# Kernel tuning notes

Measured on AMD Instinct MI355X. Metric: run time of the kernel, lower is better.

## Reference

```python
import jax, jax.numpy as jnp
import numpy as np

B, S = 16, 8192
Q_DIM, K_DIM, ATTN_DIM = 512, 512, 512


def setup_inputs() -> dict:
    key = jax.random.key(0)
    k1, k2, k3, k4, k5, k6 = jax.random.split(key, 6)
    query = jax.random.normal(k1, (B, Q_DIM), dtype=jnp.float32)
    keys = jax.random.normal(k2, (B, S, K_DIM), dtype=jnp.float32)
    mask = jax.random.randint(k3, (B, S), 0, 2, dtype=jnp.int32)
    # learned params (torch Linear stores weight as [out, in]; we keep [in, out])
    Wq = jax.random.normal(k4, (Q_DIM, ATTN_DIM), dtype=jnp.float32) / np.sqrt(Q_DIM)
    Wk = jax.random.normal(k5, (K_DIM, ATTN_DIM), dtype=jnp.float32) / np.sqrt(K_DIM)
    v = jax.random.normal(k6, (ATTN_DIM,), dtype=jnp.float32) / np.sqrt(ATTN_DIM)
    return {"query": query, "keys": keys, "mask": mask, "Wq": Wq, "Wk": Wk, "v": v}


def reference(query, keys, mask, Wq, Wk, v):
    # q: [B, 1, A], k: [B, S, A]
    q = (query @ Wq)[:, None, :]
    k = jnp.einsum('bsk,ka->bsa', keys, Wk)
    # scores e: [B, S]  (v-projection reduces attn dim)
    e = jnp.einsum('bsa,a->bs', jnp.tanh(q + k), v)
    neg_min = jnp.finfo(e.dtype).min
    e = jnp.where(mask == 0, neg_min, e)
    a = jax.nn.softmax(e, axis=-1)  # [B, S]
    c = jnp.einsum('bs,bsk->bk', a, keys)  # context [B, K_DIM]
    return (c, a)
```

## Files before the change

kernel.cpp:

```cpp
#include <hip/hip_runtime.h>

#define BB 16
#define SS 8192
#define DD 512

typedef float  f32x4  __attribute__((ext_vector_type(4)));
typedef __bf16 bf16x8 __attribute__((ext_vector_type(8)));
typedef __bf16 bf16x4 __attribute__((ext_vector_type(4)));

__device__ __forceinline__ void cvt_store_bf4(unsigned short* dst, f32x4 v) {
    bf16x4 o;
    o.x = (__bf16)v.x; o.y = (__bf16)v.y; o.z = (__bf16)v.z; o.w = (__bf16)v.w;
    *(bf16x4*)dst = o;
}

__device__ __forceinline__ float tanh_fast(float x) {
    float e2 = __expf(2.0f * x);
    return 1.0f - 2.0f / (e2 + 1.0f);
}

__global__ void prep_kernel(const float* __restrict__ query, const float* __restrict__ Wq,
                            const float* __restrict__ Wk, float* __restrict__ qproj,
                            unsigned short* __restrict__ WkT)
{
    const int bid = blockIdx.x, t = threadIdx.x;
    if (bid < DD) {
        const int n = bid;
        for (int k = t; k < DD; k += 256) {
            __bf16 h = (__bf16)Wk[k * DD + n];
            WkT[n * DD + k] = __builtin_bit_cast(unsigned short, h);
        }
    } else {
        const int idx = (bid - DD) * 256 + t;
        const int b = idx >> 9;
        const int n = idx & 511;
        const float* q  = query + b * DD;
        const float* wp = Wq + n;
        float acc = 0.0f;
#pragma unroll 8
        for (int k = 0; k < DD; ++k)
            acc = fmaf(q[k], wp[(size_t)k * DD], acc);
        qproj[b * DD + n] = acc;
    }
}

__global__ __launch_bounds__(256, 2) void fused_kernel(
    const float* __restrict__ keys, const unsigned short* __restrict__ WkT,
    const float* __restrict__ qproj, const float* __restrict__ vvec,
    const int* __restrict__ mask, float* __restrict__ e_ws,
    float* __restrict__ cpart, float2* __restrict__ ml_ws)
{
    __shared__ unsigned short ksA[16 * 2048];
    __shared__ float sm_part[4][64];
    __shared__ float w_sh[64];
    __shared__ f32x4 red[128];

    const int tid  = threadIdx.x;
    const int w    = tid >> 6;
    const int lane = tid & 63;
    const int ml   = lane & 15;
    const int quad = lane >> 4;
    const int bid  = blockIdx.x;
    const int b    = bid >> 7;
    const int chunk = bid & 127;
    const int s0   = chunk << 6;

    const int m  = tid >> 2;
    const int q4 = tid & 3;
    const float* krow = keys + ((size_t)(b * SS + s0 + m)) * DD + q4 * 4;
    const int it  = m >> 4;
    const int g0  = q4 >> 1;
    const int j0  = (q4 & 1) * 4;
    const int base0 = it * 512 + ((m & 15) + 16 * g0)       * 8 + j0;
    const int base1 = it * 512 + ((m & 15) + 16 * (g0 + 2)) * 8 + j0;
#pragma unroll 4
    for (int j = 0; j < 16; ++j) {
        f32x4 k0 = *(const f32x4*)(krow + j * 32);
        f32x4 k1 = *(const f32x4*)(krow + j * 32 + 16);
        cvt_store_bf4(&ksA[j * 2048 + base0], k0);
        cvt_store_bf4(&ksA[j * 2048 + base1], k1);
    }
    __syncthreads();

    const unsigned short* wb = WkT + (size_t)(w * 128 + ml) * DD + quad * 8;

    f32x4 acc[4][8];
#pragma unroll
    for (int i = 0; i < 4; ++i)
#pragma unroll
        for (int jn = 0; jn < 8; ++jn) acc[i][jn] = (f32x4){0.f, 0.f, 0.f, 0.f};

#pragma unroll 2
    for (int j = 0; j < 16; ++j) {
        bf16x8 af[4];
#pragma unroll
        for (int i = 0; i < 4; ++i)
            af[i] = *(const bf16x8*)&ksA[j * 2048 + (i * 64 + lane) * 8];
#pragma unroll
        for (int jn = 0; jn < 8; ++jn) {
            bf16x8 bfr = *(const bf16x8*)(wb + (size_t)jn * 16 * DD + j * 32);
#pragma unroll
            for (int i = 0; i < 4; ++i)
                acc[i][jn] = __builtin_amdgcn_mfma_f32_16x16x32_bf16(af[i], bfr, acc[i][jn], 0, 0, 0);
        }
    }

    float qv[8], vv[8];
#pragma unroll
    for (int jn = 0; jn < 8; ++jn) {
        const int n = w * 128 + jn * 16 + ml;
        qv[jn] = qproj[b * DD + n];
        vv[jn] = vvec[n];
    }
#pragma unroll
    for (int i = 0; i < 4; ++i) {
#pragma unroll
        for (int r = 0; r < 4; ++r) {
            float s = 0.0f;
#pragma unroll
            for (int jn = 0; jn < 8; ++jn) {
                float xx = acc[i][jn][r] + qv[jn];
                s += tanh_fast(xx) * vv[jn];
            }
            s += __shfl_xor(s, 1, 64);
            s += __shfl_xor(s, 2, 64);
            s += __shfl_xor(s, 4, 64);
            s += __shfl_xor(s, 8, 64);
            if (ml == 0) sm_part[w][i * 16 + quad * 4 + r] = s;
        }
    }
    __syncthreads();

    if (tid < 64) {
        float e = sm_part[0][tid] + sm_part[1][tid] + sm_part[2][tid] + sm_part[3][tid];
        const int mk = mask[b * SS + s0 + tid];
        if (mk == 0) e = -3.402823466e38f;
        e_ws[(size_t)b * SS + s0 + tid] = e;
        float mx = e;
#pragma unroll
        for (int off = 32; off >= 1; off >>= 1) mx = fmaxf(mx, __shfl_xor(mx, off, 64));
        float wv = (mk == 0) ? 0.0f : __expf(e - mx);
        float l  = wv;
#pragma unroll
        for (int off = 32; off >= 1; off >>= 1) l += __shfl_xor(l, off, 64);
        w_sh[tid] = wv;
        if (tid == 0) ml_ws[b * 128 + chunk] = make_float2(mx, l);
    }
    __syncthreads();

    const int n4 = (tid & 127) << 2;
    const int sh = tid >> 7;
    const float* kctx = keys + ((size_t)(b * SS + s0 + sh * 32)) * DD + n4;
    f32x4 cacc = (f32x4){0.f, 0.f, 0.f, 0.f};
#pragma unroll 8
    for (int sI = 0; sI < 32; ++sI) {
        float wgt = w_sh[sh * 32 + sI];
        f32x4 kv  = *(const f32x4*)(kctx + (size_t)sI * DD);
        cacc += kv * wgt;
    }
    if (sh == 1) red[tid & 127] = cacc;
    __syncthreads();
    if (sh == 0) {
        cacc += red[tid];
        *(f32x4*)(cpart + ((size_t)(b * 128 + chunk)) * 512 + n4) = cacc;
    }
}

__global__ __launch_bounds__(256) void finalize_kernel(
    const float* __restrict__ e_ws, const float* __restrict__ cpart,
    const float2* __restrict__ ml_ws, float* __restrict__ out)
{
    __shared__ float rm[4], rs[4];
    __shared__ float sc_sh[128];
    const int bid = blockIdx.x, t = threadIdx.x;
    const int b = (bid < 16) ? bid : ((bid - 16) >> 3);

    float mi = -3.402823466e38f, li = 0.0f;
    if (t < 128) { float2 p = ml_ws[b * 128 + t]; mi = p.x; li = p.y; }
    float mr = mi;
#pragma unroll
    for (int off = 32; off >= 1; off >>= 1) mr = fmaxf(mr, __shfl_xor(mr, off, 64));
    if ((t & 63) == 0) rm[t >> 6] = mr;
    __syncthreads();
    const float M = fmaxf(fmaxf(rm[0], rm[1]), fmaxf(rm[2], rm[3]));
    float si = (t < 128) ? li * __expf(mi - M) : 0.0f;
#pragma unroll
    for (int off = 32; off >= 1; off >>= 1) si += __shfl_xor(si, off, 64);
    if ((t & 63) == 0) rs[t >> 6] = si;
    __syncthreads();
    const float L = rs[0] + rs[1] + rs[2] + rs[3];
    const float invL = 1.0f / L;

    if (bid < 16) {
        if (t < 128) sc_sh[t] = __expf(ml_ws[b * 128 + t].x - M);
        __syncthreads();
        const int n0 = t * 2;
        float a0 = 0.0f, a1 = 0.0f;
#pragma unroll 4
        for (int i = 0; i < 128; ++i) {
            const float sc = sc_sh[i];
            const float* cp = cpart + ((size_t)(b * 128 + i)) * 512 + n0;
            a0 = fmaf(cp[0], sc, a0);
            a1 = fmaf(cp[1], sc, a1);
        }
        out[b * DD + n0]     = a0 * invL;
        out[b * DD + n0 + 1] = a1 * invL;
    } else {
        const int chunk8 = (bid - 16) & 7;
        const float* ep = e_ws + (size_t)b * SS + chunk8 * 1024;
        float* ap = out + BB * DD + (size_t)b * SS + chunk8 * 1024;
#pragma unroll
        for (int r = 0; r < 4; ++r) {
            float e = ep[t + 256 * r];
            ap[t + 256 * r] = __expf(e - M) * invL;
        }
    }
}

extern "C" void kernel_launch(void* const* d_in, const int* in_sizes, int n_in,
                              void* d_out, int out_size, void* d_ws, size_t ws_size,
                              hipStream_t stream)
{
    const float* query = (const float*)d_in[0];
    const float* keys  = (const float*)d_in[1];
    const int*   mask  = (const int*)  d_in[2];
    const float* Wq    = (const float*)d_in[3];
    const float* Wk    = (const float*)d_in[4];
    const float* v     = (const float*)d_in[5];
    float* out = (float*)d_out;

    float*          qproj = (float*)d_ws;
    unsigned short* WkT   = (unsigned short*)((char*)d_ws + 32768);
    float*          e_ws  = (float*)((char*)d_ws + 32768 + 524288);
    float*          cpart = (float*)((char*)d_ws + 32768 + 2 * 524288);
    float2*         ml_ws = (float2*)((char*)d_ws + 32768 + 2 * 524288 + 4194304);

    prep_kernel    <<<DD + 32, 256, 0, stream>>>(query, Wq, Wk, qproj, WkT);
    fused_kernel   <<<BB * (SS / 64), 256, 0, stream>>>(keys, WkT, qproj, v, mask,
                                                        e_ws, cpart, ml_ws);
    finalize_kernel<<<16 + 128, 256, 0, stream>>>(e_ws, cpart, ml_ws, out);
}
```

Baseline: 560.4 us.

## Widen fused kernel to 512 threads, tile Wk transpose, split finalize reduction

The fused kernel moves from 256 to 512 threads per block, with eight waves each taking 64 of the attention columns. This halves per-thread accumulators and adds an extra reduction stage for the scores and the context partials. The prep kernel now transposes Wk through a 64x64 LDS tile with vectorized loads and stores instead of strided per-element accesses. The finalize context reduction is split across four waves with an LDS combine. The larger blocks aim for more parallelism per block and less register pressure, at the cost of more partial-sum traffic and a declared occupancy that may not be reachable.

```diff
diff --git a/kernel.cpp b/kernel.cpp
--- a/kernel.cpp
+++ b/kernel.cpp
@@ -19,19 +19,32 @@
     return 1.0f - 2.0f / (e2 + 1.0f);
 }
 
-__global__ void prep_kernel(const float* __restrict__ query, const float* __restrict__ Wq,
-                            const float* __restrict__ Wk, float* __restrict__ qproj,
-                            unsigned short* __restrict__ WkT)
-{
+__global__ __launch_bounds__(256) void prep_kernel(
+    const float* __restrict__ query, const float* __restrict__ Wq,
+    const float* __restrict__ Wk, float* __restrict__ qproj,
+    unsigned short* __restrict__ WkT)
+{
+    __shared__ __bf16 lt[64][65];
     const int bid = blockIdx.x, t = threadIdx.x;
-    if (bid < DD) {
-        const int n = bid;
-        for (int k = t; k < DD; k += 256) {
-            __bf16 h = (__bf16)Wk[k * DD + n];
-            WkT[n * DD + k] = __builtin_bit_cast(unsigned short, h);
+    if (bid < 64) {
+        const int k0 = (bid >> 3) * 64, n0 = (bid & 7) * 64;
+#pragma unroll
+        for (int rep = 0; rep < 4; ++rep) {
+            const int k = rep * 16 + (t >> 4), n = (t & 15) * 4;
+            f32x4 vv = *(const f32x4*)&Wk[(size_t)(k0 + k) * DD + n0 + n];
+            lt[k][n] = (__bf16)vv.x; lt[k][n + 1] = (__bf16)vv.y;
+            lt[k][n + 2] = (__bf16)vv.z; lt[k][n + 3] = (__bf16)vv.w;
+        }
+        __syncthreads();
+#pragma unroll
+        for (int rep = 0; rep < 4; ++rep) {
+            const int n = rep * 16 + (t >> 4), k = (t & 15) * 4;
+            bf16x4 o;
+            o.x = lt[k][n]; o.y = lt[k + 1][n]; o.z = lt[k + 2][n]; o.w = lt[k + 3][n];
+            *(bf16x4*)&WkT[(size_t)(n0 + n) * DD + k0 + k] = o;
         }
     } else {
-        const int idx = (bid - DD) * 256 + t;
+        const int idx = (bid - 64) * 256 + t;
         const int b = idx >> 9;
         const int n = idx & 511;
         const float* q  = query + b * DD;
@@ -44,16 +57,16 @@
     }
 }
 
-__global__ __launch_bounds__(256, 2) void fused_kernel(
+__global__ __launch_bounds__(512, 4) void fused_kernel(
     const float* __restrict__ keys, const unsigned short* __restrict__ WkT,
     const float* __restrict__ qproj, const float* __restrict__ vvec,
     const int* __restrict__ mask, float* __restrict__ e_ws,
     float* __restrict__ cpart, float2* __restrict__ ml_ws)
 {
     __shared__ unsigned short ksA[16 * 2048];
-    __shared__ float sm_part[4][64];
+    __shared__ float sm_part[8][64];
     __shared__ float w_sh[64];
-    __shared__ f32x4 red[128];
+    __shared__ f32x4 red[3][128];
 
     const int tid  = threadIdx.x;
     const int w    = tid >> 6;
@@ -65,39 +78,36 @@
     const int chunk = bid & 127;
     const int s0   = chunk << 6;
 
-    const int m  = tid >> 2;
-    const int q4 = tid & 3;
-    const float* krow = keys + ((size_t)(b * SS + s0 + m)) * DD + q4 * 4;
-    const int it  = m >> 4;
-    const int g0  = q4 >> 1;
-    const int j0  = (q4 & 1) * 4;
-    const int base0 = it * 512 + ((m & 15) + 16 * g0)       * 8 + j0;
-    const int base1 = it * 512 + ((m & 15) + 16 * (g0 + 2)) * 8 + j0;
+    const int m  = tid >> 3;
+    const int q8 = tid & 7;
+    const float* krow = keys + ((size_t)(b * SS + s0 + m)) * DD + q8 * 4;
+    const int it = m >> 4;
+    const int sq = q8 >> 1;
+    const int j0 = (q8 & 1) * 4;
+    const int base = it * 512 + ((m & 15) + 16 * sq) * 8 + j0;
+#pragma unroll 8
+    for (int j = 0; j < 16; ++j) {
+        f32x4 kv = *(const f32x4*)(krow + j * 32);
+        cvt_store_bf4(&ksA[j * 2048 + base], kv);
+    }
+    __syncthreads();
+
+    const unsigned short* wb = WkT + (size_t)(w * 64 + ml) * DD + quad * 8;
+
+    f32x4 acc[4][4];
+#pragma unroll
+    for (int i = 0; i < 4; ++i)
+#pragma unroll
+        for (int jn = 0; jn < 4; ++jn) acc[i][jn] = (f32x4){0.f, 0.f, 0.f, 0.f};
+
 #pragma unroll 4
     for (int j = 0; j < 16; ++j) {
-        f32x4 k0 = *(const f32x4*)(krow + j * 32);
-        f32x4 k1 = *(const f32x4*)(krow + j * 32 + 16);
-        cvt_store_bf4(&ksA[j * 2048 + base0], k0);
-        cvt_store_bf4(&ksA[j * 2048 + base1], k1);
-    }
-    __syncthreads();
-
-    const unsigned short* wb = WkT + (size_t)(w * 128 + ml) * DD + quad * 8;
-
-    f32x4 acc[4][8];
-#pragma unroll
-    for (int i = 0; i < 4; ++i)
-#pragma unroll
-        for (int jn = 0; jn < 8; ++jn) acc[i][jn] = (f32x4){0.f, 0.f, 0.f, 0.f};
-
-#pragma unroll 2
-    for (int j = 0; j < 16; ++j) {
         bf16x8 af[4];
 #pragma unroll
         for (int i = 0; i < 4; ++i)
             af[i] = *(const bf16x8*)&ksA[j * 2048 + (i * 64 + lane) * 8];
 #pragma unroll
-        for (int jn = 0; jn < 8; ++jn) {
+        for (int jn = 0; jn < 4; ++jn) {
             bf16x8 bfr = *(const bf16x8*)(wb + (size_t)jn * 16 * DD + j * 32);
 #pragma unroll
             for (int i = 0; i < 4; ++i)
@@ -105,10 +115,10 @@
         }
     }
 
-    float qv[8], vv[8];
-#pragma unroll
-    for (int jn = 0; jn < 8; ++jn) {
-        const int n = w * 128 + jn * 16 + ml;
+    float qv[4], vv[4];
+#pragma unroll
+    for (int jn = 0; jn < 4; ++jn) {
+        const int n = w * 64 + jn * 16 + ml;
         qv[jn] = qproj[b * DD + n];
         vv[jn] = vvec[n];
     }
@@ -118,7 +128,7 @@
         for (int r = 0; r < 4; ++r) {
             float s = 0.0f;
 #pragma unroll
-            for (int jn = 0; jn < 8; ++jn) {
+            for (int jn = 0; jn < 4; ++jn) {
                 float xx = acc[i][jn][r] + qv[jn];
                 s += tanh_fast(xx) * vv[jn];
             }
@@ -132,7 +142,8 @@
     __syncthreads();
 
     if (tid < 64) {
-        float e = sm_part[0][tid] + sm_part[1][tid] + sm_part[2][tid] + sm_part[3][tid];
+        float e = sm_part[0][tid] + sm_part[1][tid] + sm_part[2][tid] + sm_part[3][tid]
+                + sm_part[4][tid] + sm_part[5][tid] + sm_part[6][tid] + sm_part[7][tid];
         const int mk = mask[b * SS + s0 + tid];
         if (mk == 0) e = -3.402823466e38f;
         e_ws[(size_t)b * SS + s0 + tid] = e;
@@ -150,18 +161,18 @@
 
     const int n4 = (tid & 127) << 2;
     const int sh = tid >> 7;
-    const float* kctx = keys + ((size_t)(b * SS + s0 + sh * 32)) * DD + n4;
+    const float* kctx = keys + ((size_t)(b * SS + s0 + sh * 16)) * DD + n4;
     f32x4 cacc = (f32x4){0.f, 0.f, 0.f, 0.f};
 #pragma unroll 8
-    for (int sI = 0; sI < 32; ++sI) {
-        float wgt = w_sh[sh * 32 + sI];
+    for (int sI = 0; sI < 16; ++sI) {
+        float wgt = w_sh[sh * 16 + sI];
         f32x4 kv  = *(const f32x4*)(kctx + (size_t)sI * DD);
         cacc += kv * wgt;
     }
-    if (sh == 1) red[tid & 127] = cacc;
+    if (sh) red[sh - 1][tid & 127] = cacc;
     __syncthreads();
     if (sh == 0) {
-        cacc += red[tid];
+        cacc += red[0][tid] + red[1][tid] + red[2][tid];
         *(f32x4*)(cpart + ((size_t)(b * 128 + chunk)) * 512 + n4) = cacc;
     }
 }
@@ -172,6 +183,7 @@
 {
     __shared__ float rm[4], rs[4];
     __shared__ float sc_sh[128];
+    __shared__ float cred[4][512];
     const int bid = blockIdx.x, t = threadIdx.x;
     const int b = (bid < 16) ? bid : ((bid - 16) >> 3);
 
@@ -194,17 +206,23 @@
     if (bid < 16) {
         if (t < 128) sc_sh[t] = __expf(ml_ws[b * 128 + t].x - M);
         __syncthreads();
-        const int n0 = t * 2;
-        float a0 = 0.0f, a1 = 0.0f;
+        const int w2 = t >> 6, l = t & 63;
+        float pa[8] = {0.f, 0.f, 0.f, 0.f, 0.f, 0.f, 0.f, 0.f};
 #pragma unroll 4
-        for (int i = 0; i < 128; ++i) {
+        for (int i = w2 * 32; i < w2 * 32 + 32; ++i) {
             const float sc = sc_sh[i];
-            const float* cp = cpart + ((size_t)(b * 128 + i)) * 512 + n0;
-            a0 = fmaf(cp[0], sc, a0);
-            a1 = fmaf(cp[1], sc, a1);
-        }
-        out[b * DD + n0]     = a0 * invL;
-        out[b * DD + n0 + 1] = a1 * invL;
+            const float* cp = cpart + ((size_t)(b * 128 + i)) * 512 + l * 8;
+#pragma unroll
+            for (int c = 0; c < 8; ++c) pa[c] = fmaf(cp[c], sc, pa[c]);
+        }
+#pragma unroll
+        for (int c = 0; c < 8; ++c) cred[w2][l * 8 + c] = pa[c];
+        __syncthreads();
+#pragma unroll
+        for (int rep = 0; rep < 2; ++rep) {
+            const int n = t + rep * 256;
+            out[b * DD + n] = (cred[0][n] + cred[1][n] + cred[2][n] + cred[3][n]) * invL;
+        }
     } else {
         const int chunk8 = (bid - 16) & 7;
         const float* ep = e_ws + (size_t)b * SS + chunk8 * 1024;
@@ -235,8 +253,8 @@
     float*          cpart = (float*)((char*)d_ws + 32768 + 2 * 524288);
     float2*         ml_ws = (float2*)((char*)d_ws + 32768 + 2 * 524288 + 4194304);
 
-    prep_kernel    <<<DD + 32, 256, 0, stream>>>(query, Wq, Wk, qproj, WkT);
-    fused_kernel   <<<BB * (SS / 64), 256, 0, stream>>>(keys, WkT, qproj, v, mask,
+    prep_kernel    <<<96, 256, 0, stream>>>(query, Wq, Wk, qproj, WkT);
+    fused_kernel   <<<BB * (SS / 64), 512, 0, stream>>>(keys, WkT, qproj, v, mask,
                                                         e_ws, cpart, ml_ws);
     finalize_kernel<<<16 + 128, 256, 0, stream>>>(e_ws, cpart, ml_ws, out);
 }
```

Measured after the change: 538.0 us. -4.0%, faster.
